# Optimization experiments

Hardware: AMD Instinct MI355X
Metric: run time of the kernel (lower is better)

Reference implementation:

```python
import jax, jax.numpy as jnp
import numpy as np

B, S, E, H = 4, 2048, 512, 8
HD = E // H  # v head dim = 64; q/k per-head dim is E (=512) per the module's d_k


def setup_inputs() -> dict:
    key = jax.random.key(0)
    ks = jax.random.split(key, 4)
    def xav(k, shape):
        fan_in, fan_out = shape
        lim = float(np.sqrt(6.0 / (fan_in + fan_out)))
        return jax.random.uniform(k, shape, jnp.float32, -lim, lim)
    return {
        "x": jax.random.normal(ks[0], (B, S, E), jnp.float32),
        "Wqk": xav(ks[1], (E, 2 * E * H)),
        "bqk": jnp.zeros((2 * E * H,), jnp.float32),
        "Wv": xav(ks[2], (E, E)),
        "bv": jnp.zeros((E,), jnp.float32),
        "Wo": xav(ks[3], (E, E)),
        "bo": jnp.zeros((E,), jnp.float32),
    }


def reference(x, Wqk, bqk, Wv, bv, Wo, bo):
    # fused q/k projection: [B,S,E] @ [E, 2*E*H] -> [B,S,H,2E] -> [B,H,S,2E]
    qk = (x @ Wqk + bqk).reshape(B, S, H, 2 * E).transpose(0, 2, 1, 3)
    q, k = qk[..., :E], qk[..., E:]            # each [B,H,S,E]
    v = (x @ Wv + bv).reshape(B, S, H, HD).transpose(0, 2, 1, 3)  # [B,H,S,HD]
    scale = 1.0 / jnp.sqrt(jnp.asarray(E, x.dtype))
    scores = jnp.einsum("bhqe,bhke->bhqk", q, k) * scale
    attn = jax.nn.softmax(scores, axis=-1)
    vals = jnp.einsum("bhqk,bhkd->bhqd", attn, v)  # [B,H,S,HD]
    vals = vals.transpose(0, 2, 1, 3).reshape(B, S, E)
    return vals @ Wo + bo
```

## Files before the change

### kernel.cpp

```cpp
#include <hip/hip_runtime.h>
#include <cstdint>
#include <cstddef>

typedef unsigned short u16;
typedef unsigned char u8;
typedef long i64;
typedef __attribute__((ext_vector_type(8))) short bh8;
typedef __attribute__((ext_vector_type(4))) float fx4;
typedef __attribute__((ext_vector_type(8))) int i32x8;

__device__ __forceinline__ u16 f2bf(float f) {
  unsigned int u = __float_as_uint(f);
  u += 0x7fffu + ((u >> 16) & 1u);
  return (u16)(u >> 16);
}

__device__ __forceinline__ u8 f2e4m3(float f) {
  unsigned int u = __float_as_uint(f);
  unsigned int s = (u >> 24) & 0x80u;
  unsigned int mag = u & 0x7fffffffu;
  mag += 0x7ffffu + ((mag >> 20) & 1u);
  if (mag < 0x3C800000u) return (u8)s;
  unsigned int e8 = (mag >> 23) - 120u;
  unsigned int m8 = (mag >> 20) & 7u;
  return (u8)(s | (e8 << 3) | m8);
}

typedef __attribute__((address_space(1))) void g1_void;
typedef __attribute__((address_space(3))) void l3_void;
__device__ __forceinline__ void gload_lds16(const void* g, const void* lds) {
  __builtin_amdgcn_global_load_lds((g1_void*)(uintptr_t)g,
                                   (l3_void*)(unsigned int)(uintptr_t)lds,
                                   16, 0, 0);
}

__device__ __forceinline__ fx4 MFMA(bh8 a, bh8 b, fx4 c) {
  return __builtin_amdgcn_mfma_f32_16x16x32_bf16(a, b, c, 0, 0, 0);
}
__device__ __forceinline__ fx4 MFMAMX(i32x8 a, i32x8 b, fx4 c) {
  return __builtin_amdgcn_mfma_scale_f32_16x16x128_f8f6f4(a, b, c, 0, 0,
                                                          0, 0x7F, 0, 0x7F);
}
__device__ __forceinline__ i32x8 mk8(uint4 lo, uint4 hi) {
  i32x8 v;
  v[0] = (int)lo.x; v[1] = (int)lo.y; v[2] = (int)lo.z; v[3] = (int)lo.w;
  v[4] = (int)hi.x; v[5] = (int)hi.y; v[6] = (int)hi.z; v[7] = (int)hi.w;
  return v;
}

__global__ void cast_x2(const float* __restrict__ in, u16* __restrict__ outb,
                        u8* __restrict__ out8) {
  int i = blockIdx.x * 256 + threadIdx.x;
  float4 f = ((const float4*)in)[i];
  ushort4 u;
  u.x = f2bf(f.x); u.y = f2bf(f.y); u.z = f2bf(f.z); u.w = f2bf(f.w);
  ((ushort4*)outb)[i] = u;
  unsigned int p = (unsigned int)f2e4m3(f.x) | ((unsigned int)f2e4m3(f.y) << 8)
                 | ((unsigned int)f2e4m3(f.z) << 16) | ((unsigned int)f2e4m3(f.w) << 24);
  ((unsigned int*)out8)[i] = p;
}

__global__ void tcast(const float* __restrict__ W, u16* __restrict__ Wt, int R, int C) {
  __shared__ float t[32][33];
  int tx = threadIdx.x, ty = threadIdx.y;
  int c0 = blockIdx.x * 32, r0 = blockIdx.y * 32;
#pragma unroll
  for (int i = 0; i < 4; i++)
    t[ty + i * 8][tx] = W[(size_t)(r0 + ty + i * 8) * C + c0 + tx];
  __syncthreads();
#pragma unroll
  for (int i = 0; i < 4; i++)
    Wt[(size_t)(c0 + ty + i * 8) * R + r0 + tx] = f2bf(t[tx][ty + i * 8]);
}

__global__ void tcast8(const float* __restrict__ W, u8* __restrict__ Wt, int R, int C) {
  __shared__ float t[32][33];
  int tx = threadIdx.x, ty = threadIdx.y;
  int c0 = blockIdx.x * 32, r0 = blockIdx.y * 32;
#pragma unroll
  for (int i = 0; i < 4; i++)
    t[ty + i * 8][tx] = W[(size_t)(r0 + ty + i * 8) * C + c0 + tx];
  __syncthreads();
#pragma unroll
  for (int i = 0; i < 4; i++)
    Wt[(size_t)(c0 + ty + i * 8) * R + r0 + tx] = f2e4m3(t[tx][ty + i * 8] * 256.0f);
}

template <int OUT_MODE>
__global__ __launch_bounds__(256) void gemm_bt(const u16* __restrict__ A,
                                               const u16* __restrict__ Bt,
                                               const float* __restrict__ bias,
                                               void* __restrict__ Cout,
                                               int M, int N, int K) {
  __shared__ u16 As[128 * 64];
  __shared__ u16 Bs[128 * 64];
  const int tid = threadIdx.x;
  const int l = tid & 63, w = tid >> 6;
  const int lane15 = l & 15, quad = l >> 4;
  const int wm = (w >> 1) * 64, wn = (w & 1) * 64;
  const int bm = blockIdx.y * 128, bn = blockIdx.x * 128;
  fx4 acc[4][4] = {};

  const int srow = w * 32 + (l >> 3);
  const int scol = ((l & 7) ^ (l >> 3)) * 8;
  const u16* Ag = A + (size_t)(bm + srow) * K + scol;
  const u16* Bg = Bt + (size_t)(bn + srow) * K + scol;

  for (int kt = 0; kt < K; kt += 64) {
    __syncthreads();
#pragma unroll
    for (int c = 0; c < 4; c++) {
      gload_lds16(Ag + (size_t)(c * 8) * K + kt, As + (w * 32 + c * 8) * 64);
      gload_lds16(Bg + (size_t)(c * 8) * K + kt, Bs + (w * 32 + c * 8) * 64);
    }
    __syncthreads();
#pragma unroll
    for (int kk8 = 0; kk8 < 8; kk8 += 4) {
      bh8 a[4], b[4];
#pragma unroll
      for (int mi = 0; mi < 4; mi++) {
        int r = wm + mi * 16 + lane15;
        a[mi] = *(const bh8*)(As + r * 64 + (((kk8 + quad) ^ (r & 7)) * 8));
      }
#pragma unroll
      for (int ni = 0; ni < 4; ni++) {
        int r = wn + ni * 16 + lane15;
        b[ni] = *(const bh8*)(Bs + r * 64 + (((kk8 + quad) ^ (r & 7)) * 8));
      }
#pragma unroll
      for (int mi = 0; mi < 4; mi++)
#pragma unroll
        for (int ni = 0; ni < 4; ni++)
          acc[mi][ni] = MFMA(a[mi], b[ni], acc[mi][ni]);
    }
  }
#pragma unroll
  for (int mi = 0; mi < 4; mi++)
#pragma unroll
    for (int ni = 0; ni < 4; ni++) {
      int col = bn + wn + ni * 16 + lane15;
      float bv = bias[col];
#pragma unroll
      for (int r = 0; r < 4; r++) {
        int row = bm + wm + mi * 16 + quad * 4 + r;
        float v = acc[mi][ni][r] + bv;
        if (OUT_MODE == 3)
          ((u16*)Cout)[((size_t)((row >> 11) * 512 + col) << 11) + (row & 2047)] = f2bf(v);
        else if (OUT_MODE == 1) ((u16*)Cout)[(size_t)row * N + col] = f2bf(v);
        else                    ((float*)Cout)[(size_t)row * N + col] = v;
      }
    }
}

__global__ __launch_bounds__(256) void gemm8_bt(const u8* __restrict__ A,
                                                const u8* __restrict__ Bt,
                                                const float* __restrict__ bias,
                                                u8* __restrict__ Cout,
                                                int M, int N, int K) {
  __shared__ u8 As[128 * 128];
  __shared__ u8 Bs[128 * 128];
  const int tid = threadIdx.x;
  const int l = tid & 63, w = tid >> 6;
  const int lane15 = l & 15, quad = l >> 4;
  const int wm = (w >> 1) * 64, wn = (w & 1) * 64;
  const int bm = blockIdx.y * 128, bn = blockIdx.x * 128;
  fx4 acc[4][4] = {};

  const int srow = w * 32 + (l >> 3);
  const int scol = ((l & 7) ^ ((l >> 3) & 7)) * 16;
  const u8* Ag = A + (size_t)(bm + srow) * K + scol;
  const u8* Bg = Bt + (size_t)(bn + srow) * K + scol;

  const int q2 = quad * 2;
  for (int kt = 0; kt < K; kt += 128) {
    __syncthreads();
#pragma unroll
    for (int c = 0; c < 4; c++) {
      gload_lds16(Ag + (size_t)(c * 8) * K + kt, As + (w * 32 + c * 8) * 128);
      gload_lds16(Bg + (size_t)(c * 8) * K + kt, Bs + (w * 32 + c * 8) * 128);
    }
    __syncthreads();
    i32x8 a[4], b[4];
#pragma unroll
    for (int mi = 0; mi < 4; mi++) {
      int r = wm + mi * 16 + lane15;
      const u8* rp = As + r * 128;
      a[mi] = mk8(*(const uint4*)(rp + ((q2 ^ (r & 7)) * 16)),
                  *(const uint4*)(rp + (((q2 + 1) ^ (r & 7)) * 16)));
    }
#pragma unroll
    for (int ni = 0; ni < 4; ni++) {
      int r = wn + ni * 16 + lane15;
      const u8* rp = Bs + r * 128;
      b[ni] = mk8(*(const uint4*)(rp + ((q2 ^ (r & 7)) * 16)),
                  *(const uint4*)(rp + (((q2 + 1) ^ (r & 7)) * 16)));
    }
#pragma unroll
    for (int mi = 0; mi < 4; mi++)
#pragma unroll
      for (int ni = 0; ni < 4; ni++)
        acc[mi][ni] = MFMAMX(a[mi], b[ni], acc[mi][ni]);
  }
#pragma unroll
  for (int mi = 0; mi < 4; mi++)
#pragma unroll
    for (int ni = 0; ni < 4; ni++) {
      int col = bn + wn + ni * 16 + lane15;
      float bv = bias[col];
#pragma unroll
      for (int r = 0; r < 4; r++) {
        int row = bm + wm + mi * 16 + quad * 4 + r;
        Cout[(size_t)row * N + col] = f2e4m3(acc[mi][ni][r] * 0.00390625f + bv);
      }
    }
}

__global__ __launch_bounds__(256, 3) void flash_attn(const u8* __restrict__ qk8,
                                                     const u16* __restrict__ vt,
                                                     u16* __restrict__ vals) {
  __shared__ __align__(16) u8 Ks[2][32 * 512];
  __shared__ __align__(16) u16 Vs[2][64 * 40];
  __shared__ __align__(16) u16 Ps[4][32 * 40];
  const int tid = threadIdx.x;
  const int l = tid & 63, w = tid >> 6;
  const int lane15 = l & 15, quad = l >> 4;
  const int q0 = blockIdx.x * 128;
  const int h = blockIdx.y, b = blockIdx.z;
  const float scale2 = 0.063762531f;
  const float Mb = 2.0f;

  i32x8 qmx[2][4];
#pragma unroll
  for (int mt = 0; mt < 2; mt++) {
    const u8* qrow = qk8 + (size_t)(b * 2048 + q0 + w * 32 + mt * 16 + lane15) * 8192
                   + h * 1024 + quad * 32;
#pragma unroll
    for (int e = 0; e < 4; e++)
      qmx[mt][e] = mk8(*(const uint4*)(qrow + e * 128),
                       *(const uint4*)(qrow + e * 128 + 16));
  }

  fx4 accO[2][4] = {};
  float lpart[2][4] = {};

  const u8* kbase = qk8 + (size_t)(b * 2048) * 8192 + h * 1024 + 512;
  const u16* vrow = vt + (size_t)((b * 8 + h) * 64 + (tid >> 2)) * 2048 + (tid & 3) * 8;
  const int vs_off = (tid >> 2) * 40 + (tid & 3) * 8;

  uint4 vreg = *(const uint4*)vrow;
#pragma unroll
  for (int c = 0; c < 4; c++) {
    int R0 = w * 8 + 2 * c;
    int r = R0 + (l >> 5);
    gload_lds16(kbase + (size_t)r * 8192 + (((l & 31) ^ (r & 7)) * 16),
                &Ks[0][R0 * 512]);
  }

  for (int t = 0; t < 64; t++) {
    const int cb = t & 1, nb = cb ^ 1;
    const int kt0 = t * 32;
    __syncthreads();

    bh8 pf0, pf1, vf0, vf1, vf2, vf3;
    if (t > 0) {
      const u16* vsb = &Vs[(t - 1) & 1][0];
      pf0 = *(const bh8*)(&Ps[w][lane15 * 40 + quad * 8]);
      pf1 = *(const bh8*)(&Ps[w][(16 + lane15) * 40 + quad * 8]);
      vf0 = *(const bh8*)(vsb + (lane15)      * 40 + quad * 8);
      vf1 = *(const bh8*)(vsb + (16 + lane15) * 40 + quad * 8);
      vf2 = *(const bh8*)(vsb + (32 + lane15) * 40 + quad * 8);
      vf3 = *(const bh8*)(vsb + (48 + lane15) * 40 + quad * 8);
    }

    *(uint4*)&Vs[cb][vs_off] = vreg;

    if (t < 63) {
#pragma unroll
      for (int c = 0; c < 4; c++) {
        int R0 = w * 8 + 2 * c;
        int r = R0 + (l >> 5);
        gload_lds16(kbase + (size_t)(kt0 + 32 + r) * 8192 + (((l & 31) ^ (r & 7)) * 16),
                    &Ks[nb][R0 * 512]);
      }
      vreg = *(const uint4*)(vrow + kt0 + 32);
    }

    if (t > 0) {
      accO[0][0] = MFMA(pf0, vf0, accO[0][0]); accO[1][0] = MFMA(pf1, vf0, accO[1][0]);
      accO[0][1] = MFMA(pf0, vf1, accO[0][1]); accO[1][1] = MFMA(pf1, vf1, accO[1][1]);
      accO[0][2] = MFMA(pf0, vf2, accO[0][2]); accO[1][2] = MFMA(pf1, vf2, accO[1][2]);
      accO[0][3] = MFMA(pf0, vf3, accO[0][3]); accO[1][3] = MFMA(pf1, vf3, accO[1][3]);
    }
    __builtin_amdgcn_sched_barrier(0);

    fx4 accS[2][2] = {};
    {
      const int xsw = lane15 & 7;
      const u8* rp0 = &Ks[cb][lane15 * 512];
      const u8* rp1 = &Ks[cb][(16 + lane15) * 512];
#pragma unroll
      for (int e = 0; e < 4; e++) {
        int c0 = e * 8 + quad * 2;
        i32x8 kb0 = mk8(*(const uint4*)(rp0 + ((c0 ^ xsw) * 16)),
                        *(const uint4*)(rp0 + (((c0 + 1) ^ xsw) * 16)));
        i32x8 kb1 = mk8(*(const uint4*)(rp1 + ((c0 ^ xsw) * 16)),
                        *(const uint4*)(rp1 + (((c0 + 1) ^ xsw) * 16)));
        accS[0][0] = MFMAMX(qmx[0][e], kb0, accS[0][0]);
        accS[1][0] = MFMAMX(qmx[1][e], kb0, accS[1][0]);
        accS[0][1] = MFMAMX(qmx[0][e], kb1, accS[0][1]);
        accS[1][1] = MFMAMX(qmx[1][e], kb1, accS[1][1]);
        __builtin_amdgcn_sched_barrier(0);
      }
    }

#pragma unroll
    for (int mt = 0; mt < 2; mt++)
#pragma unroll
      for (int r = 0; r < 4; r++) {
        float p0 = __builtin_amdgcn_exp2f(__fmaf_rn(accS[mt][0][r], scale2, -Mb));
        float p1 = __builtin_amdgcn_exp2f(__fmaf_rn(accS[mt][1][r], scale2, -Mb));
        lpart[mt][r] += p0 + p1;
        Ps[w][(mt * 16 + quad * 4 + r) * 40 + lane15]      = f2bf(p0);
        Ps[w][(mt * 16 + quad * 4 + r) * 40 + 16 + lane15] = f2bf(p1);
      }
  }

  {
    const u16* vsb = &Vs[1][0];
    bh8 pf0 = *(const bh8*)(&Ps[w][lane15 * 40 + quad * 8]);
    bh8 pf1 = *(const bh8*)(&Ps[w][(16 + lane15) * 40 + quad * 8]);
#pragma unroll
    for (int di = 0; di < 4; di++) {
      bh8 vf = *(const bh8*)(vsb + (di * 16 + lane15) * 40 + quad * 8);
      accO[0][di] = MFMA(pf0, vf, accO[0][di]);
      accO[1][di] = MFMA(pf1, vf, accO[1][di]);
    }
  }

#pragma unroll
  for (int mt = 0; mt < 2; mt++)
#pragma unroll
    for (int r = 0; r < 4; r++) {
      float s = lpart[mt][r];
      s += __shfl_xor(s, 1);
      s += __shfl_xor(s, 2);
      s += __shfl_xor(s, 4);
      s += __shfl_xor(s, 8);
      float inv = 1.0f / s;
      int row = q0 + w * 32 + mt * 16 + quad * 4 + r;
      u16* orow = vals + (size_t)(b * 2048 + row) * 512 + h * 64 + lane15;
#pragma unroll
      for (int di = 0; di < 4; di++) orow[di * 16] = f2bf(accO[mt][di][r] * inv);
    }
}

extern "C" void kernel_launch(void* const* d_in, const int* in_sizes, int n_in,
                              void* d_out, int out_size, void* d_ws, size_t ws_size,
                              hipStream_t stream) {
  const float* x   = (const float*)d_in[0];
  const float* Wqk = (const float*)d_in[1];
  const float* bqk = (const float*)d_in[2];
  const float* Wv  = (const float*)d_in[3];
  const float* bv  = (const float*)d_in[4];
  const float* Wo  = (const float*)d_in[5];
  const float* bo  = (const float*)d_in[6];
  float* out = (float*)d_out;

  char* ws = (char*)d_ws;
  u16* x_bf  = (u16*)(ws);
  u8*  x8    = (u8*)(ws + 8388608);
  u8*  wqk8  = (u8*)(ws + 12582912);
  u16* wvt   = (u16*)(ws + 16777216);
  u16* wot   = (u16*)(ws + 17301504);
  u16* vtbuf = (u16*)(ws + 17825792);
  u16* valsb = (u16*)(ws + 26214400);
  u8*  qk8   = (u8*)(ws + 34603008);

  cast_x2<<<4096, 256, 0, stream>>>(x, x_bf, x8);
  tcast8<<<dim3(256, 16), dim3(32, 8), 0, stream>>>(Wqk, wqk8, 512, 8192);
  tcast<<<dim3(16, 16),  dim3(32, 8), 0, stream>>>(Wv, wvt, 512, 512);
  tcast<<<dim3(16, 16),  dim3(32, 8), 0, stream>>>(Wo, wot, 512, 512);

  gemm8_bt<<<dim3(64, 64), 256, 0, stream>>>(x8, wqk8, bqk, qk8, 8192, 8192, 512);
  gemm_bt<3><<<dim3(4, 64), 256, 0, stream>>>(x_bf, wvt, bv, vtbuf, 8192, 512, 512);

  flash_attn<<<dim3(16, 8, 4), 256, 0, stream>>>(qk8, vtbuf, valsb);

  gemm_bt<0><<<dim3(4, 64), 256, 0, stream>>>(valsb, wot, bo, out, 8192, 512, 512);
}
```

Measured before the change: 297.8 us.

## Split attention KV range in two with atomic accumulation and separate normalize

Each attention block now covers half of the key sequence, which doubles the grid to give the GPU more parallel work. Partial unnormalized outputs and row sums go into an fp32 workspace with atomicAdd. A zeroing kernel runs before attention and a normalization kernel runs after it to produce the bf16 values. Because the softmax uses a fixed max offset, the partials can be summed without rescaling. The cost is two extra launches, extra fp32 global traffic and atomic contention.

```diff
diff --git a/kernel.cpp b/kernel.cpp
--- a/kernel.cpp
+++ b/kernel.cpp
@@ -84,6 +84,22 @@
 #pragma unroll
   for (int i = 0; i < 4; i++)
     Wt[(size_t)(c0 + ty + i * 8) * R + r0 + tx] = f2e4m3(t[tx][ty + i * 8] * 256.0f);
+}
+
+__global__ void zero_acc(float4* __restrict__ p) {
+  p[blockIdx.x * 256 + threadIdx.x] = float4{0.f, 0.f, 0.f, 0.f};
+}
+
+__global__ void norm_store(const float* __restrict__ oacc, u16* __restrict__ vals) {
+  int idx = blockIdx.x * 256 + threadIdx.x;
+  int row = idx >> 7, c4 = (idx & 127) * 4;
+  const float* rp = oacc + (size_t)row * 520;
+  float4 o = *(const float4*)(rp + c4);
+  float inv = 1.0f / rp[512 + (c4 >> 6)];
+  ushort4 u;
+  u.x = f2bf(o.x * inv); u.y = f2bf(o.y * inv);
+  u.z = f2bf(o.z * inv); u.w = f2bf(o.w * inv);
+  ((ushort4*)vals)[idx] = u;
 }
 
 template <int OUT_MODE>
@@ -217,7 +233,7 @@
 
 __global__ __launch_bounds__(256, 3) void flash_attn(const u8* __restrict__ qk8,
                                                      const u16* __restrict__ vt,
-                                                     u16* __restrict__ vals) {
+                                                     float* __restrict__ oacc) {
   __shared__ __align__(16) u8 Ks[2][32 * 512];
   __shared__ __align__(16) u16 Vs[2][64 * 40];
   __shared__ __align__(16) u16 Ps[4][32 * 40];
@@ -225,7 +241,9 @@
   const int l = tid & 63, w = tid >> 6;
   const int lane15 = l & 15, quad = l >> 4;
   const int q0 = blockIdx.x * 128;
-  const int h = blockIdx.y, b = blockIdx.z;
+  const int h = blockIdx.y;
+  const int b = blockIdx.z >> 1, sp = blockIdx.z & 1;
+  const int t0 = sp * 32;
   const float scale2 = 0.063762531f;
   const float Mb = 2.0f;
 
@@ -247,22 +265,22 @@
   const u16* vrow = vt + (size_t)((b * 8 + h) * 64 + (tid >> 2)) * 2048 + (tid & 3) * 8;
   const int vs_off = (tid >> 2) * 40 + (tid & 3) * 8;
 
-  uint4 vreg = *(const uint4*)vrow;
+  uint4 vreg = *(const uint4*)(vrow + t0 * 32);
 #pragma unroll
   for (int c = 0; c < 4; c++) {
     int R0 = w * 8 + 2 * c;
     int r = R0 + (l >> 5);
-    gload_lds16(kbase + (size_t)r * 8192 + (((l & 31) ^ (r & 7)) * 16),
+    gload_lds16(kbase + (size_t)(t0 * 32 + r) * 8192 + (((l & 31) ^ (r & 7)) * 16),
                 &Ks[0][R0 * 512]);
   }
 
-  for (int t = 0; t < 64; t++) {
+  for (int t = t0; t < t0 + 32; t++) {
     const int cb = t & 1, nb = cb ^ 1;
     const int kt0 = t * 32;
     __syncthreads();
 
     bh8 pf0, pf1, vf0, vf1, vf2, vf3;
-    if (t > 0) {
+    if (t > t0) {
       const u16* vsb = &Vs[(t - 1) & 1][0];
       pf0 = *(const bh8*)(&Ps[w][lane15 * 40 + quad * 8]);
       pf1 = *(const bh8*)(&Ps[w][(16 + lane15) * 40 + quad * 8]);
@@ -274,7 +292,7 @@
 
     *(uint4*)&Vs[cb][vs_off] = vreg;
 
-    if (t < 63) {
+    if (t < t0 + 31) {
 #pragma unroll
       for (int c = 0; c < 4; c++) {
         int R0 = w * 8 + 2 * c;
@@ -285,7 +303,7 @@
       vreg = *(const uint4*)(vrow + kt0 + 32);
     }
 
-    if (t > 0) {
+    if (t > t0) {
       accO[0][0] = MFMA(pf0, vf0, accO[0][0]); accO[1][0] = MFMA(pf1, vf0, accO[1][0]);
       accO[0][1] = MFMA(pf0, vf1, accO[0][1]); accO[1][1] = MFMA(pf1, vf1, accO[1][1]);
       accO[0][2] = MFMA(pf0, vf2, accO[0][2]); accO[1][2] = MFMA(pf1, vf2, accO[1][2]);
@@ -346,11 +364,12 @@
       s += __shfl_xor(s, 2);
       s += __shfl_xor(s, 4);
       s += __shfl_xor(s, 8);
-      float inv = 1.0f / s;
       int row = q0 + w * 32 + mt * 16 + quad * 4 + r;
-      u16* orow = vals + (size_t)(b * 2048 + row) * 512 + h * 64 + lane15;
-#pragma unroll
-      for (int di = 0; di < 4; di++) orow[di * 16] = f2bf(accO[mt][di][r] * inv);
+      float* orow = oacc + (size_t)(b * 2048 + row) * 520 + h * 64 + lane15;
+#pragma unroll
+      for (int di = 0; di < 4; di++) atomicAdd(&orow[di * 16], accO[mt][di][r]);
+      if (lane15 == 0)
+        atomicAdd(oacc + (size_t)(b * 2048 + row) * 520 + 512 + h, s);
     }
 }
 
@@ -375,6 +394,7 @@
   u16* vtbuf = (u16*)(ws + 17825792);
   u16* valsb = (u16*)(ws + 26214400);
   u8*  qk8   = (u8*)(ws + 34603008);
+  float* oacc = (float*)(ws);
 
   cast_x2<<<4096, 256, 0, stream>>>(x, x_bf, x8);
   tcast8<<<dim3(256, 16), dim3(32, 8), 0, stream>>>(Wqk, wqk8, 512, 8192);
@@ -384,7 +404,9 @@
   gemm8_bt<<<dim3(64, 64), 256, 0, stream>>>(x8, wqk8, bqk, qk8, 8192, 8192, 512);
   gemm_bt<3><<<dim3(4, 64), 256, 0, stream>>>(x_bf, wvt, bv, vtbuf, 8192, 512, 512);
 
-  flash_attn<<<dim3(16, 8, 4), 256, 0, stream>>>(qk8, vtbuf, valsb);
+  zero_acc<<<4160, 256, 0, stream>>>((float4*)oacc);
+  flash_attn<<<dim3(16, 8, 8), 256, 0, stream>>>(qk8, vtbuf, oacc);
+  norm_store<<<4096, 256, 0, stream>>>(oacc, valsb);
 
   gemm_bt<0><<<dim3(4, 64), 256, 0, stream>>>(valsb, wot, bo, out, 8192, 512, 512);
 }
```

New measurement: 491.6 us. +65.1%, slower.
